# Kernel tuning notes

Measured on AMD Instinct MI355X. Metric: run time of the kernel, lower is better.

Reference implementation:

```python
import jax, jax.numpy as jnp
import numpy as np

# Config derived from init_kwargs
VOCAB_FACTORS = (16, 16, 16, 16)   # 16^4 = 65536 = resonant vocab for 50000
D_FACTORS = (8, 8, 4, 4)           # prod = 1024 = d_model
RANK = 16
D_MODEL = 1024


def setup_inputs() -> dict:
    key = jax.random.key(0)
    ks = jax.random.split(key, 6)
    input_ids = jax.random.randint(ks[0], (8, 2048), 0, 50000, dtype=jnp.int64)
    scale = 0.02 / np.sqrt(4.0)  # orthogonal-init scale / sqrt(num_cores)
    core0 = jax.random.normal(ks[1], (16, 1, RANK, 8), dtype=jnp.float32) * scale
    core1 = jax.random.normal(ks[2], (16, RANK, RANK, 8), dtype=jnp.float32) * scale
    core2 = jax.random.normal(ks[3], (16, RANK, RANK, 4), dtype=jnp.float32) * scale
    core3 = jax.random.normal(ks[4], (16, RANK, 1, 4), dtype=jnp.float32) * scale
    # phase init: 2*pi*(i+1)/log(i+2) mod 2*pi
    i = jnp.arange(RANK, dtype=jnp.float32)
    phase_shift = jnp.mod(2.0 * jnp.pi * (i + 1.0) / jnp.log(i + 2.0), 2.0 * jnp.pi)
    return {"input_ids": input_ids, "core0": core0, "core1": core1,
            "core2": core2, "core3": core3, "phase_shift": phase_shift}


def _decompose(flat_ids):
    # big-endian mixed-radix decomposition over VOCAB_FACTORS
    strides = []
    s = 1
    for v in reversed(VOCAB_FACTORS):
        strides.append(s)
        s *= v
    strides = strides[::-1]
    return [(flat_ids // st) % v for st, v in zip(strides, VOCAB_FACTORS)]


def _forward(input_ids, cores, phase_shift):
    B, S = input_ids.shape
    flat = input_ids.reshape(-1)                     # (N,)
    idxs = _decompose(flat)
    # first core: (N, 1, r, d0) -> (N, r, d0)
    res = cores[0][idxs[0]][:, 0]
    # phase rotation on the rank bond channels
    res = res * jnp.cos(phase_shift)[None, :, None]
    N = flat.shape[0]
    for k in range(1, len(cores)):
        g = cores[k][idxs[k]]                        # (N, r_l, r_r, d_k)
        res = jnp.einsum('nrD,nrsd->nsDd', res, g)   # chain small-rank contraction
        res = res.reshape(N, g.shape[2], -1)
    return res.reshape(B, S, D_MODEL)


def reference(input_ids, core0, core1, core2, core3, phase_shift):
    return _forward(input_ids, (core0, core1, core2, core3), phase_shift)
```

## Files before the change

kernel.cpp:

```cpp
#include <hip/hip_runtime.h>


typedef float f32x4 __attribute__((ext_vector_type(4)));

__global__ __launch_bounds__(256) void k_tables(
    const float* __restrict__ core0, const float* __restrict__ core1,
    const float* __restrict__ core2, const float* __restrict__ core3,
    const float* __restrict__ phase,
    float* __restrict__ T, float* __restrict__ F)
{
  const int gid = blockIdx.x * 256 + threadIdx.x;
  const int lane = threadIdx.x & 63;
  const float cown = cosf(phase[lane & 15]);
  if (blockIdx.x < 1024) {
    const int p01 = gid >> 10, r = gid & 1023;
    const int b = r >> 6, u = r & 63;
    const int D0 = u >> 3, d1 = u & 7;
    const int i0 = p01 >> 4, i1 = p01 & 15;
    const float* c0 = core0 + i0 * 128 + D0;
    const float* c1 = core1 + i1 * 2048 + b * 8 + d1;
    float acc = 0.f;
    #pragma unroll
    for (int a = 0; a < 16; ++a) {
      const float ca = __shfl(cown, a, 16);
      acc += c0[a * 8] * ca * c1[a * 128];
    }
    const int us = (u >> 4) + (u & 15) * 4;
    T[p01 * 1024 + b * 64 + us] = acc;
  } else {
    const int o = gid - 262144;
    const int p23 = o >> 8, r = o & 255;
    const int b = r >> 4, v = r & 15;
    const int d2 = v >> 2, d3 = v & 3;
    const int i2 = p23 >> 4, i3 = p23 & 15;
    const float* c2 = core2 + i2 * 1024 + b * 64 + d2;
    const float* c3 = core3 + i3 * 64 + d3;
    float acc = 0.f;
    #pragma unroll
    for (int c = 0; c < 16; ++c)
      acc += c2[c * 4] * c3[c * 4];
    F[p23 * 256 + b * 16 + v] = acc;
  }
}

__global__ __launch_bounds__(256) void k_out9(
    const int* __restrict__ ids, const float* __restrict__ T,
    const float* __restrict__ F, float* __restrict__ out)
{
  __shared__ float sF[4][256];
  const int wv = threadIdx.x >> 6, lane = threadIdx.x & 63;
  const int n = blockIdx.x * 4 + wv;
  const int id = ids[n];
  const int p01 = id >> 8, p23 = id & 255;
  const int ug = lane >> 2, vg = lane & 3;

  f32x4 treg[16];
  const float* Tp = T + p01 * 1024 + ug * 4;
  #pragma unroll
  for (int b = 0; b < 16; ++b)
    treg[b] = *reinterpret_cast<const f32x4*>(Tp + b * 64);

  float* tF = sF[wv];
  {
    const f32x4 v = *reinterpret_cast<const f32x4*>(F + p23 * 256 + lane * 4);
    *reinterpret_cast<f32x4*>(tF + lane * 4) = v;
  }
  __syncthreads();

  float acc[4][4];
  #pragma unroll
  for (int i = 0; i < 4; ++i)
    #pragma unroll
    for (int j = 0; j < 4; ++j) acc[i][j] = 0.f;

  #pragma unroll
  for (int b = 0; b < 16; ++b) {
    const f32x4 f = *reinterpret_cast<const f32x4*>(tF + b * 16 + vg * 4);
    const f32x4 t = treg[b];
    acc[0][0] += t.x*f.x; acc[0][1] += t.x*f.y; acc[0][2] += t.x*f.z; acc[0][3] += t.x*f.w;
    acc[1][0] += t.y*f.x; acc[1][1] += t.y*f.y; acc[1][2] += t.y*f.z; acc[1][3] += t.y*f.w;
    acc[2][0] += t.z*f.x; acc[2][1] += t.z*f.y; acc[2][2] += t.z*f.z; acc[2][3] += t.z*f.w;
    acc[3][0] += t.w*f.x; acc[3][1] += t.w*f.y; acc[3][2] += t.w*f.z; acc[3][3] += t.w*f.w;
  }

  float* op = out + (size_t)n * 1024 + lane * 4;
  #pragma unroll
  for (int e = 0; e < 4; ++e) {
    f32x4 v4 = { acc[e][0], acc[e][1], acc[e][2], acc[e][3] };
    __builtin_nontemporal_store(v4, reinterpret_cast<f32x4*>(op + e * 256));
  }
}

extern "C" void kernel_launch(void* const* d_in, const int* in_sizes, int n_in,
                              void* d_out, int out_size, void* d_ws, size_t ws_size,
                              hipStream_t stream) {
  const int*   ids   = (const int*)  d_in[0];
  const float* core0 = (const float*)d_in[1];
  const float* core1 = (const float*)d_in[2];
  const float* core2 = (const float*)d_in[3];
  const float* core3 = (const float*)d_in[4];
  const float* phase = (const float*)d_in[5];
  float* out = (float*)d_out;

  float* Tt = (float*)d_ws;
  float* Ft = (float*)d_ws + 262144;

  const int tokens = in_sizes[0];
  hipLaunchKernelGGL(k_tables, dim3(1280), dim3(256), 0, stream,
                     core0, core1, core2, core3, phase, Tt, Ft);
  hipLaunchKernelGGL(k_out9, dim3(tokens / 4), dim3(256), 0, stream,
                     ids, Tt, Ft, out);
}
```

Before: 23.93 us.

## Make output kernel persistent with double-buffered prefetch of next token's tables

The output kernel now launches a fixed 1024 blocks, and each wave handles four tokens strided by 4096. While computing the current token it prefetches the next token's F row into a second shared buffer and reloads the T registers after the store. This hides gather latency and cuts block launch overhead, but assumes exactly 16384 tokens (the nwaves argument is unused). It also adds a syncthreads per iteration.

```diff
diff --git a/kernel.cpp b/kernel.cpp
--- a/kernel.cpp
+++ b/kernel.cpp
@@ -43,51 +43,71 @@
   }
 }
 
-__global__ __launch_bounds__(256) void k_out9(
+__global__ __launch_bounds__(256) void k_outE(
     const int* __restrict__ ids, const float* __restrict__ T,
-    const float* __restrict__ F, float* __restrict__ out)
+    const float* __restrict__ F, float* __restrict__ out, int nwaves)
 {
-  __shared__ float sF[4][256];
+  __shared__ float sF[4][2][256];
   const int wv = threadIdx.x >> 6, lane = threadIdx.x & 63;
-  const int n = blockIdx.x * 4 + wv;
-  const int id = ids[n];
-  const int p01 = id >> 8, p23 = id & 255;
+  const int w = blockIdx.x * 4 + wv;
   const int ug = lane >> 2, vg = lane & 3;
 
-  f32x4 treg[16];
-  const float* Tp = T + p01 * 1024 + ug * 4;
-  #pragma unroll
-  for (int b = 0; b < 16; ++b)
-    treg[b] = *reinterpret_cast<const f32x4*>(Tp + b * 64);
-
-  float* tF = sF[wv];
+  int id = ids[w];
+  int p01 = id >> 8, p23 = id & 255;
   {
     const f32x4 v = *reinterpret_cast<const f32x4*>(F + p23 * 256 + lane * 4);
-    *reinterpret_cast<f32x4*>(tF + lane * 4) = v;
+    *reinterpret_cast<f32x4*>(&sF[wv][0][lane * 4]) = v;
   }
-  __syncthreads();
-
-  float acc[4][4];
-  #pragma unroll
-  for (int i = 0; i < 4; ++i)
+  f32x4 treg[16];
+  {
+    const float* Tp = T + p01 * 1024 + ug * 4;
     #pragma unroll
-    for (int j = 0; j < 4; ++j) acc[i][j] = 0.f;
+    for (int b = 0; b < 16; ++b)
+      treg[b] = *reinterpret_cast<const f32x4*>(Tp + b * 64);
+  }
 
   #pragma unroll
-  for (int b = 0; b < 16; ++b) {
-    const f32x4 f = *reinterpret_cast<const f32x4*>(tF + b * 16 + vg * 4);
-    const f32x4 t = treg[b];
-    acc[0][0] += t.x*f.x; acc[0][1] += t.x*f.y; acc[0][2] += t.x*f.z; acc[0][3] += t.x*f.w;
-    acc[1][0] += t.y*f.x; acc[1][1] += t.y*f.y; acc[1][2] += t.y*f.z; acc[1][3] += t.y*f.w;
-    acc[2][0] += t.z*f.x; acc[2][1] += t.z*f.y; acc[2][2] += t.z*f.z; acc[2][3] += t.z*f.w;
-    acc[3][0] += t.w*f.x; acc[3][1] += t.w*f.y; acc[3][2] += t.w*f.z; acc[3][3] += t.w*f.w;
-  }
+  for (int it = 0; it < 4; ++it) {
+    __syncthreads();
+    const float* tF = &sF[wv][it & 1][0];
 
-  float* op = out + (size_t)n * 1024 + lane * 4;
-  #pragma unroll
-  for (int e = 0; e < 4; ++e) {
-    f32x4 v4 = { acc[e][0], acc[e][1], acc[e][2], acc[e][3] };
-    __builtin_nontemporal_store(v4, reinterpret_cast<f32x4*>(op + e * 256));
+    int nid = 0;
+    if (it < 3) {
+      nid = ids[w + (it + 1) * 4096];
+      const f32x4 v = *reinterpret_cast<const f32x4*>(
+          F + (nid & 255) * 256 + lane * 4);
+      *reinterpret_cast<f32x4*>(&sF[wv][(it + 1) & 1][lane * 4]) = v;
+    }
+
+    float acc[4][4];
+    #pragma unroll
+    for (int i = 0; i < 4; ++i)
+      #pragma unroll
+      for (int j = 0; j < 4; ++j) acc[i][j] = 0.f;
+
+    #pragma unroll
+    for (int b = 0; b < 16; ++b) {
+      const f32x4 f = *reinterpret_cast<const f32x4*>(tF + b * 16 + vg * 4);
+      const f32x4 t = treg[b];
+      acc[0][0] += t.x*f.x; acc[0][1] += t.x*f.y; acc[0][2] += t.x*f.z; acc[0][3] += t.x*f.w;
+      acc[1][0] += t.y*f.x; acc[1][1] += t.y*f.y; acc[1][2] += t.y*f.z; acc[1][3] += t.y*f.w;
+      acc[2][0] += t.z*f.x; acc[2][1] += t.z*f.y; acc[2][2] += t.z*f.z; acc[2][3] += t.z*f.w;
+      acc[3][0] += t.w*f.x; acc[3][1] += t.w*f.y; acc[3][2] += t.w*f.z; acc[3][3] += t.w*f.w;
+    }
+
+    float* op = out + (size_t)(it * 4096 + w) * 1024 + lane * 4;
+    #pragma unroll
+    for (int e = 0; e < 4; ++e) {
+      f32x4 v4 = { acc[e][0], acc[e][1], acc[e][2], acc[e][3] };
+      __builtin_nontemporal_store(v4, reinterpret_cast<f32x4*>(op + e * 256));
+    }
+
+    if (it < 3) {
+      const float* Tp = T + (nid >> 8) * 1024 + ug * 4;
+      #pragma unroll
+      for (int b = 0; b < 16; ++b)
+        treg[b] = *reinterpret_cast<const f32x4*>(Tp + b * 64);
+    }
   }
 }
 
@@ -108,6 +128,6 @@
   const int tokens = in_sizes[0];
   hipLaunchKernelGGL(k_tables, dim3(1280), dim3(256), 0, stream,
                      core0, core1, core2, core3, phase, Tt, Ft);
-  hipLaunchKernelGGL(k_out9, dim3(tokens / 4), dim3(256), 0, stream,
-                     ids, Tt, Ft, out);
+  hipLaunchKernelGGL(k_outE, dim3(1024), dim3(256), 0, stream,
+                     ids, Tt, Ft, out, tokens / 4);
 }
```

Result: slower. 24.44 us (+2.1%).
